# Kernel tuning notes

Measured on AMD Instinct MI355X. Metric: run time of the kernel, lower is better.

## Reference

```python
import jax, jax.numpy as jnp
import numpy as np

B, L, D, T, NL = 64, 512, 512, 5000, 2


def setup_inputs() -> dict:
    key = jax.random.key(0)
    k1, k2, k3, k4 = jax.random.split(key, 4)
    enc_output = jax.random.normal(k1, (B, L, D), dtype=jnp.float32)
    # stands in for the row/col-normalized tag co-occurrence matrix (values in [0, 0.01])
    ui_adj = jax.random.uniform(k2, (T, T), dtype=jnp.float32) * 0.01
    # one GCN weight matrix per layer in the layer_stack
    Ws = jax.random.normal(k3, (NL, D, D), dtype=jnp.float32) / np.sqrt(D).astype(np.float32)
    # event ids are 1-indexed in the original (it indexes with e - 1)
    event_type = jax.random.randint(k4, (B, L), 1, T + 1, dtype=jnp.int64)
    slf_attn_mask = jnp.zeros((B, L, L), dtype=bool)
    non_pad_mask = jnp.ones((B, L), dtype=bool)
    return {"enc_output": enc_output, "ui_adj": ui_adj, "Ws": Ws,
            "event_type": event_type, "slf_attn_mask": slf_attn_mask,
            "non_pad_mask": non_pad_mask}


def reference(enc_output, ui_adj, Ws, event_type, slf_attn_mask, non_pad_mask):
    # --- batched per-sample adjacency gather (replaces the Python loop) ---
    idx = event_type - 1                                   # [B, L] 0-indexed
    sub = ui_adj[idx[:, :, None], idx[:, None, :]]         # [B, L, L] = ui_adj[e-1,:][:, e-1]
    diag = ui_adj[idx, idx]                                # [B, L]   = ui_adj[e-1, e-1]
    adj = sub + diag[:, None, :]                           # vector broadcasts across rows, as in torch
    # --- GNN layer stack (hGCN layer ~ relu(A @ X @ W)) ---
    x = enc_output
    for l in range(Ws.shape[0]):                           # small fixed n_layers loop
        x = jax.nn.relu(jnp.einsum('bij,bjd->bid', adj, x) @ Ws[l])
    # --- mean pool over sequence ---
    return x.mean(axis=1)                                  # [B, D]
```

## Files before the change

kernel.cpp:

```cpp
#include <hip/hip_runtime.h>

typedef unsigned short u16;
typedef unsigned int u32;
typedef __bf16 bf16x8 __attribute__((ext_vector_type(8)));
typedef float f32x4 __attribute__((ext_vector_type(4)));
typedef int i32x4 __attribute__((ext_vector_type(4)));
typedef u32 u32x2 __attribute__((ext_vector_type(2)));
typedef u32 u32x4 __attribute__((ext_vector_type(4)));

#define T_ 5000
#define CAP 96

__device__ __forceinline__ u16 f2bf(float f) {
  u32 u = __float_as_uint(f);
  u += 0x7fffu + ((u >> 16) & 1u);
  return (u16)(u >> 16);
}

__device__ __forceinline__ void gload_lds16(const u16* g, u16* l) {
  __builtin_amdgcn_global_load_lds(
      (__attribute__((address_space(1))) void*)(u16*)g,
      (__attribute__((address_space(3))) void*)l, 16, 0, 0);
}

__device__ __forceinline__ u32 lds_off(const void* p) {
  return (u32)(uintptr_t)(__attribute__((address_space(3))) const void*)p;
}

__device__ __forceinline__ u32 swz(int row, int kb) {
  return (u32)((row >> 1) * 128 +
               ((((row & 1) << 6) | kb) ^ (((row >> 1) & 7) << 4)));
}

__global__ void prep_k(const float* __restrict__ src, u16* __restrict__ dst,
                       int* __restrict__ cnt) {
  __shared__ float tile[32][33];
  const int tx = threadIdx.x, ty = threadIdx.y;
  const int a0 = blockIdx.x * 32;
  const int b0 = blockIdx.y * 32;
  const size_t zoff = (size_t)blockIdx.z * (512 * 512);
  const float* s = src + zoff;
  u16* d = dst + zoff;
#pragma unroll
  for (int r = 0; r < 4; ++r)
    tile[ty + r * 8][tx] = s[(size_t)(a0 + ty + r * 8) * 512 + b0 + tx];
  const int gid = ((blockIdx.z * 16 + blockIdx.y) * 16 + blockIdx.x) * 256 + ty * 32 + tx;
  if (gid < 5008) cnt[gid] = 0;
  __syncthreads();
#pragma unroll
  for (int r = 0; r < 4; ++r)
    d[(size_t)(b0 + ty + r * 8) * 512 + a0 + tx] = f2bf(tile[tx][ty + r * 8]);
}

__global__ void fill_k(const int* __restrict__ ev, const float* __restrict__ ui,
                       int2* __restrict__ cd, int* __restrict__ cnt,
                       int* __restrict__ list, int* __restrict__ ovf) {
  const int t = blockIdx.x * 256 + threadIdx.x;
  const int r = ev[t] - 1;
  int2 v;
  v.x = r;
  v.y = __float_as_int(ui[(size_t)r * (T_ + 1)]);
  cd[t] = v;
  const int pos = atomicAdd(&cnt[r], 1);
  if (pos < CAP) list[r * CAP + pos] = t;
  else { const int o = atomicAdd(&cnt[5000], 1); ovf[o] = t; }
}

__global__ __launch_bounds__(256)
void grow_gather(const float* __restrict__ ui, const int2* __restrict__ cd,
                 const int* __restrict__ cnt, const int* __restrict__ list,
                 const int* __restrict__ ovf, u16* __restrict__ adj) {
  __shared__ float row[5000];
  __shared__ int lst[CAP];
  const int r = blockIdx.x;
  int c = cnt[r];
  if (c > CAP) c = CAP;
  const int j = threadIdx.x * 2;
  if (c > 0) {
    const float* __restrict__ src = ui + (size_t)r * T_;
    for (int t = threadIdx.x; t < 1250; t += 256)
      *(float4*)&row[t * 4] = *(const float4*)&src[t * 4];
    if (threadIdx.x < c) lst[threadIdx.x] = list[r * CAP + threadIdx.x];
    __syncthreads();
    int q = 0;
    for (; q + 4 <= c; q += 4) {
      const int t0 = lst[q], t1 = lst[q + 1], t2 = lst[q + 2], t3 = lst[q + 3];
      const int4 p0 = *(const int4*)&cd[((t0 >> 9) << 9) + j];
      const int4 p1 = *(const int4*)&cd[((t1 >> 9) << 9) + j];
      const int4 p2 = *(const int4*)&cd[((t2 >> 9) << 9) + j];
      const int4 p3 = *(const int4*)&cd[((t3 >> 9) << 9) + j];
      const u32 k0 = (u32)f2bf(row[p0.x] + __int_as_float(p0.y)) |
                     ((u32)f2bf(row[p0.z] + __int_as_float(p0.w)) << 16);
      const u32 k1 = (u32)f2bf(row[p1.x] + __int_as_float(p1.y)) |
                     ((u32)f2bf(row[p1.z] + __int_as_float(p1.w)) << 16);
      const u32 k2 = (u32)f2bf(row[p2.x] + __int_as_float(p2.y)) |
                     ((u32)f2bf(row[p2.z] + __int_as_float(p2.w)) << 16);
      const u32 k3 = (u32)f2bf(row[p3.x] + __int_as_float(p3.y)) |
                     ((u32)f2bf(row[p3.z] + __int_as_float(p3.w)) << 16);
      *(u32*)&adj[(size_t)t0 * 512 + j] = k0;
      *(u32*)&adj[(size_t)t1 * 512 + j] = k1;
      *(u32*)&adj[(size_t)t2 * 512 + j] = k2;
      *(u32*)&adj[(size_t)t3 * 512 + j] = k3;
    }
    for (; q < c; ++q) {
      const int t0 = lst[q];
      const int4 p0 = *(const int4*)&cd[((t0 >> 9) << 9) + j];
      const u32 k0 = (u32)f2bf(row[p0.x] + __int_as_float(p0.y)) |
                     ((u32)f2bf(row[p0.z] + __int_as_float(p0.w)) << 16);
      *(u32*)&adj[(size_t)t0 * 512 + j] = k0;
    }
  }
  if (r < 8) {
    const int n = cnt[5000];
    for (int q = r; q < n; q += 8) {
      const int t = ovf[q];
      const long rr = (long)cd[t].x;
      const float* __restrict__ rp = ui + rr * (long)T_;
      const int4 p = *(const int4*)&cd[((t >> 9) << 9) + j];
      const u32 pk = (u32)f2bf(rp[p.x] + __int_as_float(p.y)) |
                     ((u32)f2bf(rp[p.z] + __int_as_float(p.w)) << 16);
      *(u32*)&adj[(size_t)t * 512 + j] = pk;
    }
  }
}

template <int MODE, int BSRC>
__global__ __launch_bounds__(512, 2)
void gemm256(const u16* __restrict__ A, const void* __restrict__ Bv,
             u16* __restrict__ C, size_t strideA, size_t strideB, size_t strideC,
             float* __restrict__ P) {
  extern __shared__ u16 smem[];
  const int tid = threadIdx.x;
  const int lane = tid & 63;
  const int w = tid >> 6;
  const int wm = w >> 2, wn = w & 3;
  const int chunk = gridDim.x >> 3;
  const int wg = blockIdx.x;
  const int mapped = (wg & 7) * chunk + (wg >> 3);
  const int batch = mapped >> 2;
  const int tm = (mapped >> 1) & 1, tn = mapped & 1;
  const int m0 = tm << 8, n0 = tn << 8;
  const int r0base = (MODE == 3) ? n0 : m0;
  const int r1base = (MODE == 3) ? m0 : n0;
  const u16* __restrict__ Ab = A + (size_t)batch * strideA;

  const u16* gA[2];
  u32 ldA[2];
#pragma unroll
  for (int r = 0; r < 2; ++r) {
    const int c = r * 512 + tid;
    const int L = c * 16;
    const int pp = L >> 7;
    const int off = (L & 127) ^ ((pp & 7) << 4);
    const int m = pp * 2 + (off >> 6);
    const int kb = off & 63;
    gA[r] = Ab + (size_t)(r0base + m) * 512 + (kb >> 1);
    ldA[r] = (u32)((r * 512 + w * 64) * 8);
  }

  const u16* gB[2] = {nullptr, nullptr};
  u32 ldB[2] = {0, 0};
  if (BSRC == 0) {
    const u16* __restrict__ Bb = (const u16*)Bv + (size_t)batch * strideB;
#pragma unroll
    for (int r = 0; r < 2; ++r) {
      const int c = r * 512 + tid;
      const int L = c * 16;
      const int pp = L >> 7;
      const int off = (L & 127) ^ ((pp & 7) << 4);
      const int m = pp * 2 + (off >> 6);
      const int kb = off & 63;
      gB[r] = Bb + (size_t)(r1base + m) * 512 + (kb >> 1);
      ldB[r] = (u32)(32768 + (r * 512 + w * 64) * 8);
    }
  }

  const int dp = tid & 127;
  const int lq = tid >> 7;
  unsigned long long encB = 0;
  u32 boff0 = 0;
  u32x2 bs0[8], bs1[8];
  if (BSRC == 1) {
    encB = (unsigned long long)(uintptr_t)((const float*)Bv + (size_t)batch * strideB);
    boff0 = (u32)(((lq * 8) * 512 + r1base + dp * 2) * 4);
  }

#define BLOAD(t, S)                                                          \
  {                                                                          \
    const u32 ob = boff0 + (u32)(t) * 65536u;                                \
    _Pragma("unroll") for (int i = 0; i < 8; ++i)                            \
        asm volatile("global_load_dwordx2 %0, %1, %2"                        \
                     : "=v"(S[i])                                            \
                     : "v"(ob + (u32)i * 2048u), "s"(encB));                 \
  }

#define CONVERT_B(S)                                                         \
  {                                                                          \
    u32 wrd0[4], wrd1[4];                                                    \
    _Pragma("unroll") for (int jj = 0; jj < 4; ++jj) {                       \
      asm("v_cvt_pk_bf16_f32 %0, %1, %2"                                     \
          : "=v"(wrd0[jj]) : "v"(S[2 * jj].x), "v"(S[2 * jj + 1].x));        \
      asm("v_cvt_pk_bf16_f32 %0, %1, %2"                                     \
          : "=v"(wrd1[jj]) : "v"(S[2 * jj].y), "v"(S[2 * jj + 1].y));        \
    }                                                                        \
    const u32 by0 = (u32)dp * 128u + ((((u32)lq * 16u)) ^ (((u32)dp & 7u) << 4)); \
    const u32 by1 = (u32)dp * 128u + ((64u | ((u32)lq * 16u)) ^ (((u32)dp & 7u) << 4)); \
    u32x4 v0, v1;                                                            \
    v0.x = wrd0[0]; v0.y = wrd0[1]; v0.z = wrd0[2]; v0.w = wrd0[3];          \
    v1.x = wrd1[0]; v1.y = wrd1[1]; v1.z = wrd1[2]; v1.w = wrd1[3];          \
    *(u32x4*)((char*)smem + 65536 + by0) = v0;                               \
    *(u32x4*)((char*)smem + 65536 + by1) = v1;                               \
  }

  const int lr = lane & 15;
  const int kbB = (lane >> 4) << 4;
  u32 fOff8[8], fOff4[4];
#pragma unroll
  for (int m = 0; m < 8; ++m) fOff8[m] = swz(wm * 128 + m * 16 + lr, kbB);
#pragma unroll
  for (int n = 0; n < 4; ++n) fOff4[n] = swz(wn * 64 + n * 16 + lr, kbB);
  const u32 ldsBase = lds_off(smem);

  f32x4 acc[8][4] = {};

  auto stageA = [&](int t) {
    const u32 bo = (u32)(t & 3) * 8192;
#pragma unroll
    for (int r = 0; r < 2; ++r) gload_lds16(gA[r] + t * 32, smem + bo + ldA[r]);
  };
  auto stageB0 = [&](int t) {
    const u32 bo = (u32)(t & 3) * 8192;
#pragma unroll
    for (int r = 0; r < 2; ++r) gload_lds16(gB[r] + t * 32, smem + bo + ldB[r]);
  };

  if (BSRC == 0) {
    stageA(0); stageB0(0); stageA(1); stageB0(1); stageA(2); stageB0(2);
  } else {
    stageA(0); stageA(1); stageA(2);
    BLOAD(0, bs0); BLOAD(1, bs1);
  }

#pragma unroll
  for (int t = 0; t < 16; ++t) {
    if (BSRC == 0) {
      if (t <= 13)      asm volatile("s_waitcnt vmcnt(8)" ::: "memory");
      else if (t == 14) asm volatile("s_waitcnt vmcnt(4)" ::: "memory");
      else              asm volatile("s_waitcnt vmcnt(0)" ::: "memory");
      __builtin_amdgcn_sched_barrier(0);
      if (t + 3 < 16) { stageA(t + 3); stageB0(t + 3); }
      asm volatile("" ::: "memory");
      __builtin_amdgcn_s_barrier();
      asm volatile("" ::: "memory");
    } else {
      if (t == 0)              asm volatile("s_waitcnt vmcnt(8)" ::: "memory");
      else if (t <= 13)        asm volatile("s_waitcnt vmcnt(10)" ::: "memory");
      else if (t == 14)        asm volatile("s_waitcnt vmcnt(8)" ::: "memory");
      else                     asm volatile("s_waitcnt vmcnt(0)" ::: "memory");
      __builtin_amdgcn_sched_barrier(0);
      if (t & 1) { CONVERT_B(bs1); } else { CONVERT_B(bs0); }
      if (t + 3 < 16) stageA(t + 3);
      if (t + 2 < 16) { if (t & 1) { BLOAD(t + 2, bs1); } else { BLOAD(t + 2, bs0); } }
      asm volatile("s_waitcnt lgkmcnt(0)" ::: "memory");
      __builtin_amdgcn_s_barrier();
      asm volatile("" ::: "memory");
    }

    const u32 c0 = ldsBase + (u32)(t & 3) * 16384;
    const u32 c1 = ldsBase + 65536u + (BSRC == 0 ? (u32)(t & 3) * 16384 : 0u);
    const u32 base8 = (MODE == 3) ? c1 : c0;
    const u32 base4 = (MODE == 3) ? c0 : c1;
    i32x4 araw[8], braw[4];
#pragma unroll
    for (int m = 0; m < 8; ++m)
      asm volatile("ds_read_b128 %0, %1" : "=v"(araw[m]) : "v"(base8 + fOff8[m]));
#pragma unroll
    for (int n = 0; n < 4; ++n)
      asm volatile("ds_read_b128 %0, %1" : "=v"(braw[n]) : "v"(base4 + fOff4[n]));
    asm volatile("s_waitcnt lgkmcnt(0)" ::: "memory");
    __builtin_amdgcn_sched_barrier(0);

    __builtin_amdgcn_s_setprio(1);
#pragma unroll
    for (int m = 0; m < 8; ++m)
#pragma unroll
      for (int n = 0; n < 4; ++n)
        acc[m][n] = __builtin_amdgcn_mfma_f32_16x16x32_bf16(
            __builtin_bit_cast(bf16x8, araw[m]),
            __builtin_bit_cast(bf16x8, braw[n]), acc[m][n], 0, 0, 0);
    __builtin_amdgcn_s_setprio(0);
    asm volatile("" ::: "memory");
    __builtin_amdgcn_s_barrier();
    __builtin_amdgcn_sched_barrier(0);
  }
#undef BLOAD
#undef CONVERT_B

  u16* Cb = C + (size_t)batch * strideC;
  if (MODE == 1) {
#pragma unroll
    for (int m = 0; m < 8; ++m) {
      const int i = m0 + wm * 128 + m * 16 + (lane >> 4) * 4;
#pragma unroll
      for (int n = 0; n < 4; ++n) {
        const int d = n0 + wn * 64 + n * 16 + (lane & 15);
        const f32x4 v = acc[m][n];
        uint2 p;
        p.x = (u32)f2bf(fmaxf(v[0], 0.f)) | ((u32)f2bf(fmaxf(v[1], 0.f)) << 16);
        p.y = (u32)f2bf(fmaxf(v[2], 0.f)) | ((u32)f2bf(fmaxf(v[3], 0.f)) << 16);
        *(uint2*)&Cb[(size_t)d * 512 + i] = p;
      }
    }
  } else if (MODE == 2) {
    const int slot = tm * 2 + wm;
#pragma unroll
    for (int n = 0; n < 4; ++n) {
      float s = 0.f;
#pragma unroll
      for (int m = 0; m < 8; ++m) {
        const f32x4 v = acc[m][n];
#pragma unroll
        for (int j = 0; j < 4; ++j) s += fmaxf(v[j], 0.f);
      }
      s += __shfl_xor(s, 16);
      s += __shfl_xor(s, 32);
      if ((lane >> 4) == 0) {
        const int d = n0 + wn * 64 + n * 16 + lane;
        P[((size_t)batch * 4 + slot) * 512 + d] = s;
      }
    }
  } else {
#pragma unroll
    for (int m = 0; m < 8; ++m) {
      const int dd = m0 + wm * 128 + m * 16 + (lane >> 4) * 4;
#pragma unroll
      for (int n = 0; n < 4; ++n) {
        const int ii = n0 + wn * 64 + n * 16 + (lane & 15);
        const f32x4 v = acc[m][n];
        uint2 p;
        p.x = (u32)f2bf(v[0]) | ((u32)f2bf(v[1]) << 16);
        p.y = (u32)f2bf(v[2]) | ((u32)f2bf(v[3]) << 16);
        *(uint2*)&Cb[(size_t)ii * 512 + dd] = p;
      }
    }
  }
}

__global__ void reduce_mean(const float* __restrict__ P, float* __restrict__ out) {
  const int t = blockIdx.x * 256 + threadIdx.x;
  const int b = t >> 9, d = t & 511;
  float s = 0.f;
#pragma unroll
  for (int q = 0; q < 4; ++q) s += P[((size_t)b * 4 + q) * 512 + d];
  out[t] = s * (1.0f / 512.0f);
}

extern "C" void kernel_launch(void* const* d_in, const int* in_sizes, int n_in,
                              void* d_out, int out_size, void* d_ws, size_t ws_size,
                              hipStream_t stream) {
  const float* enc = (const float*)d_in[0];
  const float* ui  = (const float*)d_in[1];
  const float* Ws  = (const float*)d_in[2];
  const int*   ev  = (const int*)d_in[3];
  float* out = (float*)d_out;

  char* ws = (char*)d_ws;
  const size_t SLAB = (size_t)64 * 512 * 512 * 2;
  u16* adj  = (u16*)(ws);
  u16* tbuf = (u16*)(ws + SLAB);
  u16* xb   = (u16*)(ws + 2 * SLAB);
  char* p = ws + 3 * SLAB;
  u16* wst  = (u16*)p;  p += (size_t)2 * 512 * 512 * 2;
  int2* cd  = (int2*)p; p += (size_t)32768 * 8;
  int* cnt  = (int*)p;  p += 5008 * 4;
  int* list = (int*)p;  p += (size_t)5000 * CAP * 4;
  int* ovf  = (int*)p;  p += (size_t)32768 * 4;
  float* P  = (float*)p;

  const size_t PS = (size_t)512 * 512;
  const size_t SMEM0 = 131072;
  const size_t SMEM1 = 81920;
  (void)hipFuncSetAttribute(reinterpret_cast<const void*>(gemm256<3, 1>),
                            hipFuncAttributeMaxDynamicSharedMemorySize, (int)SMEM1);
  (void)hipFuncSetAttribute(reinterpret_cast<const void*>(gemm256<1, 0>),
                            hipFuncAttributeMaxDynamicSharedMemorySize, (int)SMEM0);
  (void)hipFuncSetAttribute(reinterpret_cast<const void*>(gemm256<3, 0>),
                            hipFuncAttributeMaxDynamicSharedMemorySize, (int)SMEM0);
  (void)hipFuncSetAttribute(reinterpret_cast<const void*>(gemm256<2, 0>),
                            hipFuncAttributeMaxDynamicSharedMemorySize, (int)SMEM0);

  prep_k<<<dim3(16, 16, 2), dim3(32, 8), 0, stream>>>(Ws, wst, cnt);
  fill_k<<<128, 256, 0, stream>>>(ev, ui, cd, cnt, list, ovf);
  grow_gather<<<5000, 256, 0, stream>>>(ui, cd, cnt, list, ovf, adj);
  gemm256<3, 1><<<256, 512, SMEM1, stream>>>(adj, enc, tbuf, PS, PS, PS, nullptr);
  gemm256<1, 0><<<256, 512, SMEM0, stream>>>(tbuf, wst, xb, PS, 0, PS, nullptr);
  gemm256<3, 0><<<256, 512, SMEM0, stream>>>(adj, xb, tbuf, PS, PS, PS, nullptr);
  gemm256<2, 0><<<256, 512, SMEM0, stream>>>(tbuf, wst + PS, nullptr, PS, 0, 0, P);
  reduce_mean<<<128, 256, 0, stream>>>(P, out);
}
```

Baseline: 142.6 us.

## Fuse adjacency GEMM and weight GEMM per layer into one row-stripe kernel

Replaces the four separate 256x256-tile GEMM launches with two fused per-layer kernels. Each workgroup handles a 64-row stripe of one batch: it computes adj_stripe @ X into LDS, then multiplies that tile by W and applies relu or pooling, so the intermediate never goes to global memory. This removes the intermediate write and read and two launches. The cost is that every stripe reloads the full X and W matrices, which multiplies their L2 traffic, and the larger LDS footprint may reduce occupancy.

```diff
diff --git a/kernel.cpp b/kernel.cpp
--- a/kernel.cpp
+++ b/kernel.cpp
@@ -124,159 +124,157 @@
   }
 }
 
-template <int MODE, int BSRC>
+template <int LAYER>
 __global__ __launch_bounds__(512, 2)
-void gemm256(const u16* __restrict__ A, const void* __restrict__ Bv,
-             u16* __restrict__ C, size_t strideA, size_t strideB, size_t strideC,
-             float* __restrict__ P) {
+void fused_layer(const u16* __restrict__ adjG, const void* __restrict__ Xv,
+                 const u16* __restrict__ wstL, void* __restrict__ outp) {
   extern __shared__ u16 smem[];
   const int tid = threadIdx.x;
   const int lane = tid & 63;
   const int w = tid >> 6;
-  const int wm = w >> 2, wn = w & 3;
-  const int chunk = gridDim.x >> 3;
   const int wg = blockIdx.x;
-  const int mapped = (wg & 7) * chunk + (wg >> 3);
-  const int batch = mapped >> 2;
-  const int tm = (mapped >> 1) & 1, tn = mapped & 1;
-  const int m0 = tm << 8, n0 = tn << 8;
-  const int r0base = (MODE == 3) ? n0 : m0;
-  const int r1base = (MODE == 3) ? m0 : n0;
-  const u16* __restrict__ Ab = A + (size_t)batch * strideA;
-
-  const u16* gA[2];
-  u32 ldA[2];
-#pragma unroll
-  for (int r = 0; r < 2; ++r) {
-    const int c = r * 512 + tid;
-    const int L = c * 16;
+  const int mapped = (wg & 7) * 64 + (wg >> 3);
+  const int batch = mapped >> 3;
+  const int stripe = mapped & 7;
+  const size_t PS = (size_t)512 * 512;
+  const u16* __restrict__ adjB = adjG + (size_t)batch * PS + (size_t)(stripe * 64) * 512;
+
+  const int lr = lane & 15;
+  const int kbB = (lane >> 4) << 4;
+  const u32 ldsB = lds_off(smem);
+
+  u32 bigSrc[4], bigDstE[4];
+#pragma unroll
+  for (int r = 0; r < 4; ++r) {
+    const int cc = r * 512 + tid;
+    const int L = cc * 16;
     const int pp = L >> 7;
     const int off = (L & 127) ^ ((pp & 7) << 4);
-    const int m = pp * 2 + (off >> 6);
-    const int kb = off & 63;
-    gA[r] = Ab + (size_t)(r0base + m) * 512 + (kb >> 1);
-    ldA[r] = (u32)((r * 512 + w * 64) * 8);
-  }
-
-  const u16* gB[2] = {nullptr, nullptr};
-  u32 ldB[2] = {0, 0};
-  if (BSRC == 0) {
-    const u16* __restrict__ Bb = (const u16*)Bv + (size_t)batch * strideB;
-#pragma unroll
-    for (int r = 0; r < 2; ++r) {
-      const int c = r * 512 + tid;
-      const int L = c * 16;
-      const int pp = L >> 7;
-      const int off = (L & 127) ^ ((pp & 7) << 4);
-      const int m = pp * 2 + (off >> 6);
-      const int kb = off & 63;
-      gB[r] = Bb + (size_t)(r1base + m) * 512 + (kb >> 1);
-      ldB[r] = (u32)(32768 + (r * 512 + w * 64) * 8);
-    }
-  }
-
-  const int dp = tid & 127;
-  const int lq = tid >> 7;
+    const int row = pp * 2 + (off >> 6);
+    bigSrc[r] = (u32)(row * 512 + ((off & 63) >> 1));
+    bigDstE[r] = (u32)(32768 + (r * 512 + w * 64) * 8);
+  }
+  u32 adjSrc, adjDstE;
+  {
+    const int cc = w * 32 + (lane & 31);
+    const int L = cc * 16;
+    const int pp = L >> 7;
+    const int off = (L & 127) ^ ((pp & 7) << 4);
+    const int row = pp * 2 + (off >> 6);
+    adjSrc = (u32)(row * 512 + ((off & 63) >> 1));
+    adjDstE = (u32)(65536 + w * 256);
+  }
+
   unsigned long long encB = 0;
   u32 boff0 = 0;
-  u32x2 bs0[8], bs1[8];
-  if (BSRC == 1) {
-    encB = (unsigned long long)(uintptr_t)((const float*)Bv + (size_t)batch * strideB);
-    boff0 = (u32)(((lq * 8) * 512 + r1base + dp * 2) * 4);
-  }
-
-#define BLOAD(t, S)                                                          \
+  u32x2 bs0[16], bs1[16];
+  if (LAYER == 0) {
+    encB = (unsigned long long)(uintptr_t)((const float*)Xv + (size_t)batch * PS);
+    boff0 = (u32)((tid & 255) * 8 + (tid >> 8) * 32768);
+  }
+  const u16* __restrict__ xbS =
+      (LAYER == 1) ? ((const u16*)Xv + (size_t)batch * PS) : (const u16*)nullptr;
+
+#define BLOAD16(t, S)                                                        \
   {                                                                          \
     const u32 ob = boff0 + (u32)(t) * 65536u;                                \
-    _Pragma("unroll") for (int i = 0; i < 8; ++i)                            \
+    _Pragma("unroll") for (int i = 0; i < 16; ++i)                           \
         asm volatile("global_load_dwordx2 %0, %1, %2"                        \
-                     : "=v"(S[i])                                            \
-                     : "v"(ob + (u32)i * 2048u), "s"(encB));                 \
-  }
-
-#define CONVERT_B(S)                                                         \
+                     : "=v"(S[i]) : "v"(ob + (u32)i * 2048u), "s"(encB));    \
+  }
+
+#define CONV16(S)                                                            \
   {                                                                          \
-    u32 wrd0[4], wrd1[4];                                                    \
-    _Pragma("unroll") for (int jj = 0; jj < 4; ++jj) {                       \
-      asm("v_cvt_pk_bf16_f32 %0, %1, %2"                                     \
-          : "=v"(wrd0[jj]) : "v"(S[2 * jj].x), "v"(S[2 * jj + 1].x));        \
-      asm("v_cvt_pk_bf16_f32 %0, %1, %2"                                     \
-          : "=v"(wrd1[jj]) : "v"(S[2 * jj].y), "v"(S[2 * jj + 1].y));        \
+    u32 we_[8], wo_[8];                                                      \
+    _Pragma("unroll") for (int j = 0; j < 4; ++j) {                          \
+      asm("v_cvt_pk_bf16_f32 %0, %1, %2" : "=v"(we_[j])                      \
+          : "v"(S[2 * j].x), "v"(S[2 * j + 1].x));                           \
+      asm("v_cvt_pk_bf16_f32 %0, %1, %2" : "=v"(we_[4 + j])                  \
+          : "v"(S[8 + 2 * j].x), "v"(S[9 + 2 * j].x));                       \
+      asm("v_cvt_pk_bf16_f32 %0, %1, %2" : "=v"(wo_[j])                      \
+          : "v"(S[2 * j].y), "v"(S[2 * j + 1].y));                           \
+      asm("v_cvt_pk_bf16_f32 %0, %1, %2" : "=v"(wo_[4 + j])                  \
+          : "v"(S[8 + 2 * j].y), "v"(S[9 + 2 * j].y));                       \
     }                                                                        \
-    const u32 by0 = (u32)dp * 128u + ((((u32)lq * 16u)) ^ (((u32)dp & 7u) << 4)); \
-    const u32 by1 = (u32)dp * 128u + ((64u | ((u32)lq * 16u)) ^ (((u32)dp & 7u) << 4)); \
-    u32x4 v0, v1;                                                            \
-    v0.x = wrd0[0]; v0.y = wrd0[1]; v0.z = wrd0[2]; v0.w = wrd0[3];          \
-    v1.x = wrd1[0]; v1.y = wrd1[1]; v1.z = wrd1[2]; v1.w = wrd1[3];          \
-    *(u32x4*)((char*)smem + 65536 + by0) = v0;                               \
-    *(u32x4*)((char*)smem + 65536 + by1) = v1;                               \
-  }
-
-  const int lr = lane & 15;
-  const int kbB = (lane >> 4) << 4;
-  u32 fOff8[8], fOff4[4];
-#pragma unroll
-  for (int m = 0; m < 8; ++m) fOff8[m] = swz(wm * 128 + m * 16 + lr, kbB);
-#pragma unroll
-  for (int n = 0; n < 4; ++n) fOff4[n] = swz(wn * 64 + n * 16 + lr, kbB);
-  const u32 ldsBase = lds_off(smem);
-
-  f32x4 acc[8][4] = {};
-
-  auto stageA = [&](int t) {
-    const u32 bo = (u32)(t & 3) * 8192;
-#pragma unroll
-    for (int r = 0; r < 2; ++r) gload_lds16(gA[r] + t * 32, smem + bo + ldA[r]);
+    const int p_ = tid & 255;                                                \
+    const u32 X_ = (u32)((p_ & 7) << 4);                                     \
+    const u32 lh_ = (u32)(tid >> 8) * 32u;                                   \
+    char* rb_ = (char*)smem + 65536 + p_ * 128;                              \
+    u32x4 v_;                                                                \
+    v_.x = we_[0]; v_.y = we_[1]; v_.z = we_[2]; v_.w = we_[3];              \
+    *(u32x4*)(rb_ + (lh_ ^ X_)) = v_;                                        \
+    v_.x = we_[4]; v_.y = we_[5]; v_.z = we_[6]; v_.w = we_[7];              \
+    *(u32x4*)(rb_ + ((lh_ + 16) ^ X_)) = v_;                                 \
+    v_.x = wo_[0]; v_.y = wo_[1]; v_.z = wo_[2]; v_.w = wo_[3];              \
+    *(u32x4*)(rb_ + ((64 + lh_) ^ X_)) = v_;                                 \
+    v_.x = wo_[4]; v_.y = wo_[5]; v_.z = wo_[6]; v_.w = wo_[7];              \
+    *(u32x4*)(rb_ + ((64 + lh_ + 16) ^ X_)) = v_;                            \
+  }
+
+  auto stageBig = [&](const u16* src, int t, int buf) {
+#pragma unroll
+    for (int r = 0; r < 4; ++r)
+      gload_lds16(src + bigSrc[r] + t * 32, smem + bigDstE[r] + buf * 16384);
   };
-  auto stageB0 = [&](int t) {
-    const u32 bo = (u32)(t & 3) * 8192;
-#pragma unroll
-    for (int r = 0; r < 2; ++r) gload_lds16(gB[r] + t * 32, smem + bo + ldB[r]);
+  auto stageAdj = [&](int t, int buf) {
+    if (lane < 32)
+      gload_lds16(adjB + adjSrc + t * 32, smem + adjDstE + buf * 2048);
   };
 
-  if (BSRC == 0) {
-    stageA(0); stageB0(0); stageA(1); stageB0(1); stageA(2); stageB0(2);
+  const int wmA = w >> 1, wnA = w & 1;
+  u32 xOffA[8], adjOffA[2];
+#pragma unroll
+  for (int mf = 0; mf < 8; ++mf)
+    xOffA[mf] = 65536u + swz(wmA * 128 + mf * 16 + lr, kbB);
+#pragma unroll
+  for (int nf = 0; nf < 2; ++nf)
+    adjOffA[nf] = 131072u + swz(wnA * 32 + nf * 16 + lr, kbB);
+  const int weB = w >> 1, wiB = w & 1;
+  u32 wOffB[8], tRowB[2], tXB[2];
+#pragma unroll
+  for (int nf = 0; nf < 8; ++nf)
+    wOffB[nf] = 65536u + swz(weB * 128 + nf * 16 + lr, kbB);
+#pragma unroll
+  for (int mf = 0; mf < 2; ++mf) {
+    const int rowT = wiB * 32 + mf * 16 + lr;
+    tRowB[mf] = (u32)(rowT * 1024);
+    tXB[mf] = (u32)((rowT & 7) << 4);
+  }
+
+  f32x4 accA[8][2] = {};
+  if (LAYER == 0) {
+    BLOAD16(0, bs0); stageAdj(0, 0);
+    BLOAD16(1, bs1); stageAdj(1, 1);
   } else {
-    stageA(0); stageA(1); stageA(2);
-    BLOAD(0, bs0); BLOAD(1, bs1);
+    stageBig(xbS, 0, 0); stageAdj(0, 0);
+    stageBig(xbS, 1, 1); stageAdj(1, 1);
   }
 
 #pragma unroll
   for (int t = 0; t < 16; ++t) {
-    if (BSRC == 0) {
-      if (t <= 13)      asm volatile("s_waitcnt vmcnt(8)" ::: "memory");
-      else if (t == 14) asm volatile("s_waitcnt vmcnt(4)" ::: "memory");
-      else              asm volatile("s_waitcnt vmcnt(0)" ::: "memory");
-      __builtin_amdgcn_sched_barrier(0);
-      if (t + 3 < 16) { stageA(t + 3); stageB0(t + 3); }
-      asm volatile("" ::: "memory");
-      __builtin_amdgcn_s_barrier();
-      asm volatile("" ::: "memory");
+    if (t <= 14) {
+      if (LAYER == 0) asm volatile("s_waitcnt vmcnt(17)" ::: "memory");
+      else            asm volatile("s_waitcnt vmcnt(5)" ::: "memory");
     } else {
-      if (t == 0)              asm volatile("s_waitcnt vmcnt(8)" ::: "memory");
-      else if (t <= 13)        asm volatile("s_waitcnt vmcnt(10)" ::: "memory");
-      else if (t == 14)        asm volatile("s_waitcnt vmcnt(8)" ::: "memory");
-      else                     asm volatile("s_waitcnt vmcnt(0)" ::: "memory");
-      __builtin_amdgcn_sched_barrier(0);
-      if (t & 1) { CONVERT_B(bs1); } else { CONVERT_B(bs0); }
-      if (t + 3 < 16) stageA(t + 3);
-      if (t + 2 < 16) { if (t & 1) { BLOAD(t + 2, bs1); } else { BLOAD(t + 2, bs0); } }
+      asm volatile("s_waitcnt vmcnt(0)" ::: "memory");
+    }
+    __builtin_amdgcn_sched_barrier(0);
+    if (LAYER == 0) {
+      if (t & 1) { CONV16(bs1); } else { CONV16(bs0); }
       asm volatile("s_waitcnt lgkmcnt(0)" ::: "memory");
-      __builtin_amdgcn_s_barrier();
-      asm volatile("" ::: "memory");
-    }
-
-    const u32 c0 = ldsBase + (u32)(t & 3) * 16384;
-    const u32 c1 = ldsBase + 65536u + (BSRC == 0 ? (u32)(t & 3) * 16384 : 0u);
-    const u32 base8 = (MODE == 3) ? c1 : c0;
-    const u32 base4 = (MODE == 3) ? c0 : c1;
-    i32x4 araw[8], braw[4];
+    }
+    __builtin_amdgcn_s_barrier();
+    asm volatile("" ::: "memory");
+
+    const u32 xb_ = ldsB + ((LAYER == 1) ? (u32)(t & 1) * 32768u : 0u);
+    const u32 ab_ = ldsB + (u32)(t & 1) * 4096u;
+    i32x4 xr[8], ar2[2];
 #pragma unroll
     for (int m = 0; m < 8; ++m)
-      asm volatile("ds_read_b128 %0, %1" : "=v"(araw[m]) : "v"(base8 + fOff8[m]));
-#pragma unroll
-    for (int n = 0; n < 4; ++n)
-      asm volatile("ds_read_b128 %0, %1" : "=v"(braw[n]) : "v"(base4 + fOff4[n]));
+      asm volatile("ds_read_b128 %0, %1" : "=v"(xr[m]) : "v"(xb_ + xOffA[m]));
+#pragma unroll
+    for (int n = 0; n < 2; ++n)
+      asm volatile("ds_read_b128 %0, %1" : "=v"(ar2[n]) : "v"(ab_ + adjOffA[n]));
     asm volatile("s_waitcnt lgkmcnt(0)" ::: "memory");
     __builtin_amdgcn_sched_barrier(0);
 
@@ -284,66 +282,111 @@
 #pragma unroll
     for (int m = 0; m < 8; ++m)
 #pragma unroll
-      for (int n = 0; n < 4; ++n)
-        acc[m][n] = __builtin_amdgcn_mfma_f32_16x16x32_bf16(
-            __builtin_bit_cast(bf16x8, araw[m]),
-            __builtin_bit_cast(bf16x8, braw[n]), acc[m][n], 0, 0, 0);
+      for (int n = 0; n < 2; ++n)
+        accA[m][n] = __builtin_amdgcn_mfma_f32_16x16x32_bf16(
+            __builtin_bit_cast(bf16x8, xr[m]),
+            __builtin_bit_cast(bf16x8, ar2[n]), accA[m][n], 0, 0, 0);
     __builtin_amdgcn_s_setprio(0);
     asm volatile("" ::: "memory");
     __builtin_amdgcn_s_barrier();
     __builtin_amdgcn_sched_barrier(0);
-  }
-#undef BLOAD
-#undef CONVERT_B
-
-  u16* Cb = C + (size_t)batch * strideC;
-  if (MODE == 1) {
-#pragma unroll
-    for (int m = 0; m < 8; ++m) {
-      const int i = m0 + wm * 128 + m * 16 + (lane >> 4) * 4;
-#pragma unroll
-      for (int n = 0; n < 4; ++n) {
-        const int d = n0 + wn * 64 + n * 16 + (lane & 15);
-        const f32x4 v = acc[m][n];
+    if (t + 2 < 16) {
+      if (LAYER == 0) { if (t & 1) { BLOAD16(t + 2, bs1); } else { BLOAD16(t + 2, bs0); } }
+      else stageBig(xbS, t + 2, t & 1);
+      stageAdj(t + 2, t & 1);
+    }
+  }
+
+#pragma unroll
+  for (int nf = 0; nf < 2; ++nf)
+#pragma unroll
+    for (int mf = 0; mf < 8; ++mf) {
+      const int ii = wnA * 32 + nf * 16 + lr;
+      const int dd = wmA * 128 + mf * 16 + (lane >> 4) * 4;
+      const f32x4 v = accA[mf][nf];
+      uint2 p;
+      p.x = (u32)f2bf(v[0]) | ((u32)f2bf(v[1]) << 16);
+      p.y = (u32)f2bf(v[2]) | ((u32)f2bf(v[3]) << 16);
+      *(uint2*)((char*)smem + ii * 1024 + ((dd * 2) ^ ((ii & 7) << 4))) = p;
+    }
+  __syncthreads();
+  __builtin_amdgcn_sched_barrier(0);
+
+  f32x4 accB[2][8] = {};
+  stageBig(wstL, 0, 0);
+  stageBig(wstL, 1, 1);
+
+#pragma unroll
+  for (int t = 0; t < 16; ++t) {
+    if (t <= 14) asm volatile("s_waitcnt vmcnt(4)" ::: "memory");
+    else         asm volatile("s_waitcnt vmcnt(0)" ::: "memory");
+    __builtin_amdgcn_sched_barrier(0);
+    __builtin_amdgcn_s_barrier();
+    asm volatile("" ::: "memory");
+
+    const u32 wb_ = ldsB + (u32)(t & 1) * 32768u;
+    i32x4 tr[2], wr8[8];
+#pragma unroll
+    for (int mf = 0; mf < 2; ++mf) {
+      const u32 byt = ldsB + tRowB[mf] + (((u32)(t * 64) + (u32)kbB) ^ tXB[mf]);
+      asm volatile("ds_read_b128 %0, %1" : "=v"(tr[mf]) : "v"(byt));
+    }
+#pragma unroll
+    for (int nf = 0; nf < 8; ++nf)
+      asm volatile("ds_read_b128 %0, %1" : "=v"(wr8[nf]) : "v"(wb_ + wOffB[nf]));
+    asm volatile("s_waitcnt lgkmcnt(0)" ::: "memory");
+    __builtin_amdgcn_sched_barrier(0);
+
+    __builtin_amdgcn_s_setprio(1);
+#pragma unroll
+    for (int mf = 0; mf < 2; ++mf)
+#pragma unroll
+      for (int nf = 0; nf < 8; ++nf)
+        accB[mf][nf] = __builtin_amdgcn_mfma_f32_16x16x32_bf16(
+            __builtin_bit_cast(bf16x8, tr[mf]),
+            __builtin_bit_cast(bf16x8, wr8[nf]), accB[mf][nf], 0, 0, 0);
+    __builtin_amdgcn_s_setprio(0);
+    asm volatile("" ::: "memory");
+    __builtin_amdgcn_s_barrier();
+    __builtin_amdgcn_sched_barrier(0);
+    if (t + 2 < 16) stageBig(wstL, t + 2, t & 1);
+  }
+
+  if (LAYER == 0) {
+    u16* __restrict__ xbO = (u16*)outp + (size_t)batch * PS;
+#pragma unroll
+    for (int mf = 0; mf < 2; ++mf)
+#pragma unroll
+      for (int nf = 0; nf < 8; ++nf) {
+        const int e = weB * 128 + nf * 16 + lr;
+        const int iloc = wiB * 32 + mf * 16 + (lane >> 4) * 4;
+        const f32x4 v = accB[mf][nf];
         uint2 p;
         p.x = (u32)f2bf(fmaxf(v[0], 0.f)) | ((u32)f2bf(fmaxf(v[1], 0.f)) << 16);
         p.y = (u32)f2bf(fmaxf(v[2], 0.f)) | ((u32)f2bf(fmaxf(v[3], 0.f)) << 16);
-        *(uint2*)&Cb[(size_t)d * 512 + i] = p;
+        *(uint2*)&xbO[(size_t)e * 512 + stripe * 64 + iloc] = p;
       }
-    }
-  } else if (MODE == 2) {
-    const int slot = tm * 2 + wm;
-#pragma unroll
-    for (int n = 0; n < 4; ++n) {
+  } else {
+    float* __restrict__ Pp = (float*)outp;
+#pragma unroll
+    for (int nf = 0; nf < 8; ++nf) {
       float s = 0.f;
 #pragma unroll
-      for (int m = 0; m < 8; ++m) {
-        const f32x4 v = acc[m][n];
+      for (int mf = 0; mf < 2; ++mf) {
+        const f32x4 v = accB[mf][nf];
 #pragma unroll
         for (int j = 0; j < 4; ++j) s += fmaxf(v[j], 0.f);
       }
       s += __shfl_xor(s, 16);
       s += __shfl_xor(s, 32);
       if ((lane >> 4) == 0) {
-        const int d = n0 + wn * 64 + n * 16 + lane;
-        P[((size_t)batch * 4 + slot) * 512 + d] = s;
+        const int e = weB * 128 + nf * 16 + lane;
+        Pp[((size_t)(batch * 16 + stripe * 2 + wiB)) * 512 + e] = s;
       }
     }
-  } else {
-#pragma unroll
-    for (int m = 0; m < 8; ++m) {
-      const int dd = m0 + wm * 128 + m * 16 + (lane >> 4) * 4;
-#pragma unroll
-      for (int n = 0; n < 4; ++n) {
-        const int ii = n0 + wn * 64 + n * 16 + (lane & 15);
-        const f32x4 v = acc[m][n];
-        uint2 p;
-        p.x = (u32)f2bf(v[0]) | ((u32)f2bf(v[1]) << 16);
-        p.y = (u32)f2bf(v[2]) | ((u32)f2bf(v[3]) << 16);
-        *(uint2*)&Cb[(size_t)ii * 512 + dd] = p;
-      }
-    }
-  }
+  }
+#undef BLOAD16
+#undef CONV16
 }
 
 __global__ void reduce_mean(const float* __restrict__ P, float* __restrict__ out) {
@@ -351,7 +394,7 @@
   const int b = t >> 9, d = t & 511;
   float s = 0.f;
 #pragma unroll
-  for (int q = 0; q < 4; ++q) s += P[((size_t)b * 4 + q) * 512 + d];
+  for (int q = 0; q < 16; ++q) s += P[((size_t)b * 16 + q) * 512 + d];
   out[t] = s * (1.0f / 512.0f);
 }
 
@@ -366,10 +409,9 @@
 
   char* ws = (char*)d_ws;
   const size_t SLAB = (size_t)64 * 512 * 512 * 2;
-  u16* adj  = (u16*)(ws);
-  u16* tbuf = (u16*)(ws + SLAB);
-  u16* xb   = (u16*)(ws + 2 * SLAB);
-  char* p = ws + 3 * SLAB;
+  u16* adj = (u16*)(ws);
+  u16* xb  = (u16*)(ws + SLAB);
+  char* p = ws + 2 * SLAB;
   u16* wst  = (u16*)p;  p += (size_t)2 * 512 * 512 * 2;
   int2* cd  = (int2*)p; p += (size_t)32768 * 8;
   int* cnt  = (int*)p;  p += 5008 * 4;
@@ -378,23 +420,16 @@
   float* P  = (float*)p;
 
   const size_t PS = (size_t)512 * 512;
-  const size_t SMEM0 = 131072;
-  const size_t SMEM1 = 81920;
-  (void)hipFuncSetAttribute(reinterpret_cast<const void*>(gemm256<3, 1>),
-                            hipFuncAttributeMaxDynamicSharedMemorySize, (int)SMEM1);
-  (void)hipFuncSetAttribute(reinterpret_cast<const void*>(gemm256<1, 0>),
-                            hipFuncAttributeMaxDynamicSharedMemorySize, (int)SMEM0);
-  (void)hipFuncSetAttribute(reinterpret_cast<const void*>(gemm256<3, 0>),
-                            hipFuncAttributeMaxDynamicSharedMemorySize, (int)SMEM0);
-  (void)hipFuncSetAttribute(reinterpret_cast<const void*>(gemm256<2, 0>),
-                            hipFuncAttributeMaxDynamicSharedMemorySize, (int)SMEM0);
+  const size_t SMEM = 139264;
+  (void)hipFuncSetAttribute(reinterpret_cast<const void*>(fused_layer<0>),
+                            hipFuncAttributeMaxDynamicSharedMemorySize, (int)SMEM);
+  (void)hipFuncSetAttribute(reinterpret_cast<const void*>(fused_layer<1>),
+                            hipFuncAttributeMaxDynamicSharedMemorySize, (int)SMEM);
 
   prep_k<<<dim3(16, 16, 2), dim3(32, 8), 0, stream>>>(Ws, wst, cnt);
   fill_k<<<128, 256, 0, stream>>>(ev, ui, cd, cnt, list, ovf);
   grow_gather<<<5000, 256, 0, stream>>>(ui, cd, cnt, list, ovf, adj);
-  gemm256<3, 1><<<256, 512, SMEM1, stream>>>(adj, enc, tbuf, PS, PS, PS, nullptr);
-  gemm256<1, 0><<<256, 512, SMEM0, stream>>>(tbuf, wst, xb, PS, 0, PS, nullptr);
-  gemm256<3, 0><<<256, 512, SMEM0, stream>>>(adj, xb, tbuf, PS, PS, PS, nullptr);
-  gemm256<2, 0><<<256, 512, SMEM0, stream>>>(tbuf, wst + PS, nullptr, PS, 0, 0, P);
+  fused_layer<0><<<512, 512, SMEM, stream>>>(adj, enc, wst, xb);
+  fused_layer<1><<<512, 512, SMEM, stream>>>(adj, xb, wst + PS, P);
   reduce_mean<<<128, 256, 0, stream>>>(P, out);
 }
```

Result: slower. 163.9 us (+14.9%).
